# Kernel tuning notes

Measured on AMD Instinct MI355X. Metric: run time of the kernel, lower is better.

## Reference

```python
import jax, jax.numpy as jnp
import numpy as np

B, N_KP, DIM, STEP = 262144, 11, 2, 4


def setup_inputs() -> dict:
    key = jax.random.key(0)
    k1, k2, k3 = jax.random.split(key, 3)
    index = jnp.arange(N_KP, dtype=jnp.int32) * STEP  # keypoint frame indices [0,4,...,40]
    value = jax.random.normal(k1, (B, N_KP, DIM), dtype=jnp.float32)
    init_speed = jax.random.normal(k2, (B, 1, DIM), dtype=jnp.float32)
    init_acc = jax.random.normal(k3, (B, 1, DIM), dtype=jnp.float32)
    return {"index": index, "value": value, "init_speed": init_speed, "init_acc": init_acc}


def _interp(x, value, init_speed, init_acc):
    # x: concrete numpy int array of keypoint indices (static).
    # Closed form of the piecewise recurrence acc+=da; v+=acc; y+=v:
    #   acc_k = a0 + k*da
    #   v_k   = v0 + k*a0 + da*k(k+1)/2
    #   y_k   = y0 + k*v0 + a0*k(k+1)/2 + da*k(k+1)(k+2)/6
    # and torch's denominator n(n+1)/4 + n(n+1)(2n+1)/12 == n(n+1)(n+2)/6.
    v0, a0 = init_speed, init_acc
    outs = []
    for i in range(len(x) - 1):
        n = int(x[i + 1] - x[i])
        y0 = value[..., i:i + 1, :]
        y1 = value[..., i + 1:i + 2, :]
        dy = y1 - y0
        if n <= 1:
            outs.append(y1)
            new_v = y1 - y0
            a0 = new_v - v0
            v0 = new_v
            continue
        da = (dy - n * v0 - (n * (n + 1) / 2) * a0) / (n * (n + 1) * (n + 2) / 6)
        k = jnp.arange(1, n + 1, dtype=value.dtype)[:, None]  # (n, 1)
        # broadcast (n,1) against (..., 1, dim) -> (..., n, dim)
        pos = y0 + k * v0 + (k * (k + 1) / 2) * a0 + (k * (k + 1) * (k + 2) / 6) * da
        outs.append(pos)
        v0 = v0 + n * a0 + (n * (n + 1) / 2) * da
        a0 = a0 + n * da
    return jnp.concatenate(outs, axis=-2)  # (..., m, dim)


def reference(index, value, init_speed, init_acc):
    x = np.asarray(jax.device_get(index)).astype(np.int64)  # static keypoint indices
    return _interp(x, value, init_speed, init_acc)
```

## Files before the change

### kernel.cpp

```cpp
#include <hip/hip_runtime.h>


typedef float f4 __attribute__((ext_vector_type(4)));

template <int NSEG>
__global__ __launch_bounds__(256) void interp_kernel(
    const int* __restrict__ index,
    const float2* __restrict__ value,
    const float2* __restrict__ vinit,
    const float2* __restrict__ ainit,
    float2* __restrict__ out,
    int B, int rows, int pad2)
{
    constexpr int NKP = NSEG + 1;
    extern __shared__ char smem[];
    float2* inv = (float2*)smem;
    float2* ivi = (float2*)(smem + 64 * NKP * 8);
    float2* iai = (float2*)(smem + 64 * NKP * 8 + 512);
    float2* outt = (float2*)smem;

    int tid = threadIdx.x;
    int first_b = blockIdx.x * 64;
    int nb = B - first_b;
    if (nb > 64) nb = 64;
    bool full = (nb == 64);

    if (full) {
        const f4* gv4 = (const f4*)(value + (long)first_b * NKP);
        f4* l4 = (f4*)inv;
        constexpr int NV4 = 64 * NKP / 2;
        for (int f = tid; f < NV4; f += 256) l4[f] = gv4[f];
        if (tid < 32) {
            ((f4*)ivi)[tid] = ((const f4*)(vinit + first_b))[tid];
        } else if (tid < 64) {
            ((f4*)iai)[tid - 32] = ((const f4*)(ainit + first_b))[tid - 32];
        }
    } else {
        for (int f = tid; f < nb * NKP; f += 256) inv[f] = value[(long)first_b * NKP + f];
        if (tid < nb) ivi[tid] = vinit[first_b + tid];
        else if (tid < 2 * nb) iai[tid - nb] = ainit[first_b + tid - nb];
    }
    __syncthreads();

    int bl = tid >> 2;
    int r  = tid & 3;
    bool active = (bl < nb);

    float2 y[NKP];
    float2 v0, a0;
    int xi[NKP];
#pragma unroll
    for (int i = 0; i < NKP; ++i) xi[i] = index[i];
    if (active) {
#pragma unroll
        for (int i = 0; i < NKP; ++i) y[i] = inv[bl * NKP + i];
        v0 = ivi[bl];
        a0 = iai[bl];
    } else {
        v0 = a0 = make_float2(0.f, 0.f);
#pragma unroll
        for (int i = 0; i < NKP; ++i) y[i] = make_float2(0.f, 0.f);
    }
    __syncthreads();

    if (active) {
        float2* __restrict__ lrow = outt + bl * pad2;
        int off = 0;
#pragma unroll
        for (int i = 0; i < NSEG; ++i) {
            float2 y0 = y[i];
            float2 y1 = y[i + 1];
            int n = xi[i + 1] - xi[i];
            float dyx = y1.x - y0.x;
            float dyy = y1.y - y0.y;

            if (n <= 1) {
                if (r == 0) lrow[off] = y1;
                off += 1;
                a0.x = dyx - v0.x;
                a0.y = dyy - v0.y;
                v0.x = dyx;
                v0.y = dyy;
            } else {
                float fn = (float)n;
                float c1 = fn * (fn + 1.0f) * 0.5f;
                float c2 = fn * (fn + 1.0f) * (fn + 2.0f) / 6.0f;
                float rc2 = __builtin_amdgcn_rcpf(c2);
                float dax = (dyx - fn * v0.x - c1 * a0.x) * rc2;
                float day = (dyy - fn * v0.y - c1 * a0.y) * rc2;

                for (int k = r + 1; k <= n; k += 4) {
                    float fk = (float)k;
                    float t2 = fk * (fk + 1.0f) * 0.5f;
                    float t3 = fk * (fk + 1.0f) * (fk + 2.0f) * (1.0f / 6.0f);
                    float2 p;
                    p.x = y0.x + fk * v0.x + t2 * a0.x + t3 * dax;
                    p.y = y0.y + fk * v0.y + t2 * a0.y + t3 * day;
                    lrow[off + k - 1] = p;
                }
                off += n;

                v0.x += fn * a0.x + c1 * dax;
                v0.y += fn * a0.y + c1 * day;
                a0.x += fn * dax;
                a0.y += fn * day;
            }
        }
    }
    __syncthreads();

    if (full && (rows & 1) == 0) {
        int rowf4 = rows >> 1;
        int padf4 = pad2 >> 1;
        const f4* __restrict__ l4 = (const f4*)outt;
        f4* __restrict__ o4 = (f4*)(out + (long)first_b * rows);
        int total4 = 64 * rowf4;
        int bb = tid / rowf4;
        int j  = tid - bb * rowf4;
        int stepb = 256 / rowf4;
        int stepj = 256 - stepb * rowf4;
        for (int f = tid; f < total4; f += 256) {
            __builtin_nontemporal_store(l4[bb * padf4 + j], &o4[f]);
            j += stepj; bb += stepb;
            if (j >= rowf4) { j -= rowf4; ++bb; }
        }
    } else if (nb > 0) {
        int total2 = nb * rows;
        float2* __restrict__ o2 = out + (long)first_b * rows;
        for (int f = tid; f < total2; f += 256) {
            int bb = f / rows;
            int j  = f - bb * rows;
            o2[f] = outt[bb * pad2 + j];
        }
    }
}

__global__ __launch_bounds__(256) void interp_kernel_gen(
    const int* __restrict__ index,
    const float2* __restrict__ value,
    const float2* __restrict__ vinit,
    const float2* __restrict__ ainit,
    float2* __restrict__ out,
    int B, int nkp, int rows, int pad2)
{
    extern __shared__ char smem[];
    float2* lds = (float2*)smem;
    int tid = threadIdx.x;
    int gid = blockIdx.x * 256 + tid;
    int b  = gid >> 2;
    int r  = gid & 3;
    int bl = tid >> 2;

    if (b < B) {
        const float2* __restrict__ vrow = value + (long)b * nkp;
        float2* __restrict__ lrow = lds + bl * pad2;
        float2 v0 = vinit[b];
        float2 a0 = ainit[b];
        float2 y0 = vrow[0];
        int x0 = index[0];
        int off = 0;
        for (int i = 0; i < nkp - 1; ++i) {
            float2 y1 = vrow[i + 1];
            int x1 = index[i + 1];
            int n = x1 - x0; x0 = x1;
            float dyx = y1.x - y0.x, dyy = y1.y - y0.y;
            if (n <= 1) {
                if (r == 0) lrow[off] = y1;
                off += 1;
                a0.x = dyx - v0.x; a0.y = dyy - v0.y;
                v0.x = dyx; v0.y = dyy;
            } else {
                float fn = (float)n;
                float c1 = fn * (fn + 1.0f) * 0.5f;
                float c2 = fn * (fn + 1.0f) * (fn + 2.0f) / 6.0f;
                float dax = (dyx - fn * v0.x - c1 * a0.x) / c2;
                float day = (dyy - fn * v0.y - c1 * a0.y) / c2;
                for (int k = r + 1; k <= n; k += 4) {
                    float fk = (float)k;
                    float t2 = fk * (fk + 1.0f) * 0.5f;
                    float t3 = fk * (fk + 1.0f) * (fk + 2.0f) * (1.0f / 6.0f);
                    float2 p;
                    p.x = y0.x + fk * v0.x + t2 * a0.x + t3 * dax;
                    p.y = y0.y + fk * v0.y + t2 * a0.y + t3 * day;
                    lrow[off + k - 1] = p;
                }
                off += n;
                v0.x += fn * a0.x + c1 * dax;
                v0.y += fn * a0.y + c1 * day;
                a0.x += fn * dax;
                a0.y += fn * day;
            }
            y0 = y1;
        }
    }

    __syncthreads();

    int first_b = blockIdx.x * 64;
    int nb = B - first_b;
    if (nb > 64) nb = 64;
    if (nb <= 0) return;
    int total2 = nb * rows;
    float2* __restrict__ o2 = out + (long)first_b * rows;
    for (int f = tid; f < total2; f += 256) {
        int bb = f / rows;
        int j  = f - bb * rows;
        o2[f] = lds[bb * pad2 + j];
    }
}

extern "C" void kernel_launch(void* const* d_in, const int* in_sizes, int n_in,
                              void* d_out, int out_size, void* d_ws, size_t ws_size,
                              hipStream_t stream) {
    const int*    index = (const int*)d_in[0];
    const float2* value = (const float2*)d_in[1];
    const float2* vinit = (const float2*)d_in[2];
    const float2* ainit = (const float2*)d_in[3];
    float2*       out   = (float2*)d_out;

    int nkp  = in_sizes[0];
    int B    = in_sizes[1] / (nkp * 2);
    int rows = out_size / (B * 2);

    int pad2 = rows + 2;
    size_t smem_out = (size_t)64 * pad2 * sizeof(float2);
    size_t smem_in  = (size_t)64 * nkp * sizeof(float2) + 1024;
    size_t smem = smem_out > smem_in ? smem_out : smem_in;

    dim3 grid((B + 63) / 64);

    if (nkp == 11) {
        interp_kernel<10><<<grid, 256, smem, stream>>>(index, value, vinit, ainit, out, B, rows, pad2);
    } else {
        interp_kernel_gen<<<grid, 256, smem, stream>>>(index, value, vinit, ainit, out, B, nkp, rows, pad2);
    }
}
```

Before: 23.89 us.

## Process multiple tiles per block with register-prefetched next-tile inputs

The specialized kernel now handles four 64-row tiles per block. While the current tile is computed, the next tile's value and initial-state vectors are loaded into registers, then written to a separate LDS input region before the output write-back. This aims to hide global load latency behind compute and output stores, and to amortize block launch cost. In exchange the grid is four times smaller, LDS use per block grows, and the partial-tile fallback is moved to the generic kernel.

```diff
diff --git a/kernel.cpp b/kernel.cpp
--- a/kernel.cpp
+++ b/kernel.cpp
@@ -3,134 +3,140 @@
 
 typedef float f4 __attribute__((ext_vector_type(4)));
 
-template <int NSEG>
+template <int NSEG, int TPB>
 __global__ __launch_bounds__(256) void interp_kernel(
     const int* __restrict__ index,
     const float2* __restrict__ value,
     const float2* __restrict__ vinit,
     const float2* __restrict__ ainit,
     float2* __restrict__ out,
-    int B, int rows, int pad2)
+    int B, int rows, int pad2, int ntiles)
 {
     constexpr int NKP = NSEG + 1;
+    constexpr int NV4 = 64 * NKP / 2;
+    constexpr int NI4 = 32;
+    constexpr int NT4 = NV4 + 2 * NI4;
+
     extern __shared__ char smem[];
-    float2* inv = (float2*)smem;
-    float2* ivi = (float2*)(smem + 64 * NKP * 8);
-    float2* iai = (float2*)(smem + 64 * NKP * 8 + 512);
     float2* outt = (float2*)smem;
+    f4*     s_in = (f4*)(smem + (size_t)64 * pad2 * 8);
+    float2* inv  = (float2*)s_in;
+    float2* ivi  = (float2*)(s_in + NV4);
+    float2* iai  = (float2*)(s_in + NV4 + NI4);
 
     int tid = threadIdx.x;
-    int first_b = blockIdx.x * 64;
-    int nb = B - first_b;
-    if (nb > 64) nb = 64;
-    bool full = (nb == 64);
-
-    if (full) {
-        const f4* gv4 = (const f4*)(value + (long)first_b * NKP);
-        f4* l4 = (f4*)inv;
-        constexpr int NV4 = 64 * NKP / 2;
-        for (int f = tid; f < NV4; f += 256) l4[f] = gv4[f];
-        if (tid < 32) {
-            ((f4*)ivi)[tid] = ((const f4*)(vinit + first_b))[tid];
-        } else if (tid < 64) {
-            ((f4*)iai)[tid - 32] = ((const f4*)(ainit + first_b))[tid - 32];
-        }
-    } else {
-        for (int f = tid; f < nb * NKP; f += 256) inv[f] = value[(long)first_b * NKP + f];
-        if (tid < nb) ivi[tid] = vinit[first_b + tid];
-        else if (tid < 2 * nb) iai[tid - nb] = ainit[first_b + tid - nb];
-    }
-    __syncthreads();
-
-    int bl = tid >> 2;
-    int r  = tid & 3;
-    bool active = (bl < nb);
-
-    float2 y[NKP];
-    float2 v0, a0;
+    int bl  = tid >> 2;
+    int r   = tid & 3;
+
     int xi[NKP];
 #pragma unroll
     for (int i = 0; i < NKP; ++i) xi[i] = index[i];
-    if (active) {
+
+    int tile0 = blockIdx.x * TPB;
+    if (tile0 >= ntiles) return;
+
+    auto ld_stage = [&](int f, long fb) -> f4 {
+        if (f < NV4) return ((const f4*)(value + fb * NKP))[f];
+        else if (f < NV4 + NI4) return ((const f4*)(vinit + fb))[f - NV4];
+        else return ((const f4*)(ainit + fb))[f - NV4 - NI4];
+    };
+
+    {
+        long fb = (long)tile0 * 64;
+        f4 r0 = ld_stage(tid, fb);
+        f4 r1;
+        if (tid < NT4 - 256) r1 = ld_stage(tid + 256, fb);
+        s_in[tid] = r0;
+        if (tid < NT4 - 256) s_in[tid + 256] = r1;
+    }
+    __syncthreads();
+
+    for (int t = 0; t < TPB; ++t) {
+        int tile = tile0 + t;
+        if (tile >= ntiles) break;
+        long first_b = (long)tile * 64;
+
+        float2 y[NKP];
 #pragma unroll
         for (int i = 0; i < NKP; ++i) y[i] = inv[bl * NKP + i];
-        v0 = ivi[bl];
-        a0 = iai[bl];
-    } else {
-        v0 = a0 = make_float2(0.f, 0.f);
+        float2 v0 = ivi[bl];
+        float2 a0 = iai[bl];
+        __syncthreads();
+
+        bool more = (t + 1 < TPB) && (tile + 1 < ntiles);
+        f4 r0, r1;
+        if (more) {
+            long fb = first_b + 64;
+            r0 = ld_stage(tid, fb);
+            if (tid < NT4 - 256) r1 = ld_stage(tid + 256, fb);
+        }
+
+        {
+            float2* __restrict__ lrow = outt + bl * pad2;
+            int off = 0;
 #pragma unroll
-        for (int i = 0; i < NKP; ++i) y[i] = make_float2(0.f, 0.f);
-    }
-    __syncthreads();
-
-    if (active) {
-        float2* __restrict__ lrow = outt + bl * pad2;
-        int off = 0;
-#pragma unroll
-        for (int i = 0; i < NSEG; ++i) {
-            float2 y0 = y[i];
-            float2 y1 = y[i + 1];
-            int n = xi[i + 1] - xi[i];
-            float dyx = y1.x - y0.x;
-            float dyy = y1.y - y0.y;
-
-            if (n <= 1) {
-                if (r == 0) lrow[off] = y1;
-                off += 1;
-                a0.x = dyx - v0.x;
-                a0.y = dyy - v0.y;
-                v0.x = dyx;
-                v0.y = dyy;
-            } else {
-                float fn = (float)n;
-                float c1 = fn * (fn + 1.0f) * 0.5f;
-                float c2 = fn * (fn + 1.0f) * (fn + 2.0f) / 6.0f;
-                float rc2 = __builtin_amdgcn_rcpf(c2);
-                float dax = (dyx - fn * v0.x - c1 * a0.x) * rc2;
-                float day = (dyy - fn * v0.y - c1 * a0.y) * rc2;
-
-                for (int k = r + 1; k <= n; k += 4) {
-                    float fk = (float)k;
-                    float t2 = fk * (fk + 1.0f) * 0.5f;
-                    float t3 = fk * (fk + 1.0f) * (fk + 2.0f) * (1.0f / 6.0f);
-                    float2 p;
-                    p.x = y0.x + fk * v0.x + t2 * a0.x + t3 * dax;
-                    p.y = y0.y + fk * v0.y + t2 * a0.y + t3 * day;
-                    lrow[off + k - 1] = p;
+            for (int i = 0; i < NSEG; ++i) {
+                float2 y0 = y[i];
+                float2 y1 = y[i + 1];
+                int n = xi[i + 1] - xi[i];
+                float dyx = y1.x - y0.x;
+                float dyy = y1.y - y0.y;
+
+                if (n <= 1) {
+                    if (r == 0) lrow[off] = y1;
+                    off += 1;
+                    a0.x = dyx - v0.x;
+                    a0.y = dyy - v0.y;
+                    v0.x = dyx;
+                    v0.y = dyy;
+                } else {
+                    float fn = (float)n;
+                    float c1 = fn * (fn + 1.0f) * 0.5f;
+                    float c2 = fn * (fn + 1.0f) * (fn + 2.0f) / 6.0f;
+                    float rc2 = __builtin_amdgcn_rcpf(c2);
+                    float dax = (dyx - fn * v0.x - c1 * a0.x) * rc2;
+                    float day = (dyy - fn * v0.y - c1 * a0.y) * rc2;
+
+                    for (int k = r + 1; k <= n; k += 4) {
+                        float fk = (float)k;
+                        float t2 = fk * (fk + 1.0f) * 0.5f;
+                        float t3 = fk * (fk + 1.0f) * (fk + 2.0f) * (1.0f / 6.0f);
+                        float2 p;
+                        p.x = y0.x + fk * v0.x + t2 * a0.x + t3 * dax;
+                        p.y = y0.y + fk * v0.y + t2 * a0.y + t3 * day;
+                        lrow[off + k - 1] = p;
+                    }
+                    off += n;
+
+                    v0.x += fn * a0.x + c1 * dax;
+                    v0.y += fn * a0.y + c1 * day;
+                    a0.x += fn * dax;
+                    a0.y += fn * day;
                 }
-                off += n;
-
-                v0.x += fn * a0.x + c1 * dax;
-                v0.y += fn * a0.y + c1 * day;
-                a0.x += fn * dax;
-                a0.y += fn * day;
             }
         }
-    }
-    __syncthreads();
-
-    if (full && (rows & 1) == 0) {
-        int rowf4 = rows >> 1;
-        int padf4 = pad2 >> 1;
-        const f4* __restrict__ l4 = (const f4*)outt;
-        f4* __restrict__ o4 = (f4*)(out + (long)first_b * rows);
-        int total4 = 64 * rowf4;
-        int bb = tid / rowf4;
-        int j  = tid - bb * rowf4;
-        int stepb = 256 / rowf4;
-        int stepj = 256 - stepb * rowf4;
-        for (int f = tid; f < total4; f += 256) {
-            __builtin_nontemporal_store(l4[bb * padf4 + j], &o4[f]);
-            j += stepj; bb += stepb;
-            if (j >= rowf4) { j -= rowf4; ++bb; }
-        }
-    } else if (nb > 0) {
-        int total2 = nb * rows;
-        float2* __restrict__ o2 = out + (long)first_b * rows;
-        for (int f = tid; f < total2; f += 256) {
-            int bb = f / rows;
-            int j  = f - bb * rows;
-            o2[f] = outt[bb * pad2 + j];
+
+        if (more) {
+            s_in[tid] = r0;
+            if (tid < NT4 - 256) s_in[tid + 256] = r1;
+        }
+        __syncthreads();
+
+        {
+            int rowf4 = rows >> 1;
+            int padf4 = pad2 >> 1;
+            const f4* __restrict__ l4 = (const f4*)outt;
+            f4* __restrict__ o4 = (f4*)(out + first_b * rows);
+            int total4 = 64 * rowf4;
+            int bb = tid / rowf4;
+            int j  = tid - bb * rowf4;
+            int stepb = 256 / rowf4;
+            int stepj = 256 - stepb * rowf4;
+            for (int f = tid; f < total4; f += 256) {
+                __builtin_nontemporal_store(l4[bb * padf4 + j], &o4[f]);
+                j += stepj; bb += stepb;
+                if (j >= rowf4) { j -= rowf4; ++bb; }
+            }
         }
     }
 }
@@ -223,15 +229,19 @@
     int rows = out_size / (B * 2);
 
     int pad2 = rows + 2;
-    size_t smem_out = (size_t)64 * pad2 * sizeof(float2);
-    size_t smem_in  = (size_t)64 * nkp * sizeof(float2) + 1024;
-    size_t smem = smem_out > smem_in ? smem_out : smem_in;
-
-    dim3 grid((B + 63) / 64);
-
-    if (nkp == 11) {
-        interp_kernel<10><<<grid, 256, smem, stream>>>(index, value, vinit, ainit, out, B, rows, pad2);
+
+    if (nkp == 11 && (B % 64) == 0 && (rows % 2) == 0 && rows >= 2) {
+        constexpr int TPB = 4;
+        int ntiles = B / 64;
+        constexpr int NV4 = 64 * 11 / 2;
+        size_t smem = (size_t)64 * pad2 * 8 + (size_t)(NV4 + 64) * 16;
+        dim3 grid((ntiles + TPB - 1) / TPB);
+        interp_kernel<10, TPB><<<grid, 256, smem, stream>>>(
+            index, value, vinit, ainit, out, B, rows, pad2, ntiles);
     } else {
-        interp_kernel_gen<<<grid, 256, smem, stream>>>(index, value, vinit, ainit, out, B, nkp, rows, pad2);
+        size_t smem = (size_t)64 * pad2 * sizeof(float2);
+        dim3 grid((B + 63) / 64);
+        interp_kernel_gen<<<grid, 256, smem, stream>>>(
+            index, value, vinit, ainit, out, B, nkp, rows, pad2);
     }
 }
```

New measurement: 30.22 us. +26.5%, slower.
